# Performance work log

Measured on AMD Instinct MI355X. Metric: run time of the kernel, lower is better.

The kernel has to match this reference:

```python
import math
import jax, jax.numpy as jnp
import numpy as np

B, T, C, FC, H, L, K, WIN = 8, 512, 768, 3072, 12, 6, 3, 4
DK = C // H
SCALE = 1.0 / math.sqrt(DK)


def setup_inputs() -> dict:
    key = jax.random.key(0)
    ks = jax.random.split(key, 12)
    s = 0.02
    rn = lambda k, shape: (jax.random.normal(k, shape, jnp.float32) * s)
    rel_std = DK ** -0.5
    return {
        "x": jax.random.normal(ks[0], (B, C, T), jnp.float32),
        "x_mask": jnp.ones((B, 1, T), jnp.float32),
        "Wq": rn(ks[1], (L, C, C)), "bq": jnp.zeros((L, C), jnp.float32),
        "Wk": rn(ks[2], (L, C, C)), "bk": jnp.zeros((L, C), jnp.float32),
        "Wv": rn(ks[3], (L, C, C)), "bv": jnp.zeros((L, C), jnp.float32),
        "Wo": rn(ks[4], (L, C, C)), "bo": jnp.zeros((L, C), jnp.float32),
        "emb_rel_k": jax.random.normal(ks[5], (1, 2 * WIN + 1, DK), jnp.float32) * rel_std,
        "emb_rel_v": jax.random.normal(ks[6], (1, 2 * WIN + 1, DK), jnp.float32) * rel_std,
        "W1": rn(ks[7], (L, FC, C, K)), "b1": jnp.zeros((L, FC), jnp.float32),
        "W2": rn(ks[8], (L, C, FC, K)), "b2": jnp.zeros((L, C), jnp.float32),
        "g1": jnp.ones((L, C), jnp.float32), "be1": jnp.zeros((L, C), jnp.float32),
        "g2": jnp.ones((L, C), jnp.float32), "be2": jnp.zeros((L, C), jnp.float32),
    }


def _get_rel_emb(emb, length):
    pad = max(length - (WIN + 1), 0)
    start = max(WIN + 1 - length, 0)
    e = jnp.pad(emb, ((0, 0), (pad, pad), (0, 0)))
    return e[:, start:start + 2 * length - 1]


def _rel_to_abs(x):
    # [b,h,l,2l-1] -> [b,h,l,l]
    b, h, l, _ = x.shape
    x = jnp.pad(x, ((0, 0), (0, 0), (0, 0), (0, 1)))
    xf = x.reshape(b, h, l * 2 * l)
    xf = jnp.pad(xf, ((0, 0), (0, 0), (0, l - 1)))
    return xf.reshape(b, h, l + 1, 2 * l - 1)[:, :, :l, l - 1:]


def _abs_to_rel(x):
    # [b,h,l,l] -> [b,h,l,2l-1]
    b, h, l, _ = x.shape
    x = jnp.pad(x, ((0, 0), (0, 0), (0, 0), (0, l - 1)))
    xf = x.reshape(b, h, l * l + l * (l - 1))
    xf = jnp.pad(xf, ((0, 0), (0, 0), (l, 0)))
    return xf.reshape(b, h, l, 2 * l)[:, :, :, 1:]


def _ln(x, g, b):
    # LayerNorm over channel dim of [B,C,T]
    m = jnp.mean(x, axis=1, keepdims=True)
    v = jnp.mean(jnp.square(x - m), axis=1, keepdims=True)
    return (x - m) * jax.lax.rsqrt(v + 1e-5) * g[None, :, None] + b[None, :, None]


def _proj(x, w, b):
    # 1x1 conv == matmul over channels: x [B,C,T], w [O,C]
    return jnp.einsum('oc,bct->bot', w, x) + b[None, :, None]


def _conv1d_same(x, w, b):
    # x [B,Cin,T], w [Cout,Cin,K], same padding (pad_l=(K-1)//2, pad_r=K//2)
    k = w.shape[-1]
    out = jax.lax.conv_general_dilated(
        x, w, window_strides=(1,), padding=[((k - 1) // 2, k // 2)],
        dimension_numbers=('NCH', 'OIH', 'NCH'))
    return out + b[None, :, None]


def _heads(t):
    # [B,C,T] -> [B,H,T,DK]
    return t.reshape(B, H, DK, T).transpose(0, 1, 3, 2)


def _forward(x, x_mask, Wq, bq, Wk, bk, Wv, bv, Wo, bo, emb_rel_k, emb_rel_v,
             W1, b1, W2, b2, g1, be1, g2, be2):
    attn_mask = x_mask[:, :, None, :] * x_mask[:, :, :, None]  # [B,1,T,T]
    x = x * x_mask
    rk = _get_rel_emb(emb_rel_k, T)[0]  # [2T-1, DK]
    rv = _get_rel_emb(emb_rel_v, T)[0]
    for i in range(L):
        # --- self-attention with relative position (matmul + skew) ---
        q = _heads(_proj(x, Wq[i], bq[i]))  # [B,H,T,DK]
        k = _heads(_proj(x, Wk[i], bk[i]))
        v = _heads(_proj(x, Wv[i], bv[i]))
        qs = q * SCALE
        scores = jnp.einsum('bhtd,bhsd->bhts', qs, k)
        rel_logits = jnp.einsum('bhtd,md->bhtm', qs, rk)  # [B,H,T,2T-1]
        scores = scores + _rel_to_abs(rel_logits)
        scores = jnp.where(attn_mask == 0, -1e4, scores)
        p = jax.nn.softmax(scores, axis=-1)
        out = jnp.einsum('bhts,bhsd->bhtd', p, v)
        out = out + jnp.einsum('bhtm,md->bhtd', _abs_to_rel(p), rv)
        out = out.transpose(0, 1, 3, 2).reshape(B, C, T)
        y = _proj(out, Wo[i], bo[i])
        x = _ln(x + y, g1[i], be1[i])
        # --- conv FFN ---
        h = jax.nn.relu(_conv1d_same(x * x_mask, W1[i], b1[i]))
        y = _conv1d_same(h * x_mask, W2[i], b2[i]) * x_mask
        x = _ln(x + y, g2[i], be2[i])
    return x * x_mask


def reference(x, x_mask, Wq, bq, Wk, bk, Wv, bv, Wo, bo, emb_rel_k, emb_rel_v,
              W1, b1, W2, b2, g1, be1, g2, be2):
    return _forward(x, x_mask, Wq, bq, Wk, bk, Wv, bv, Wo, bo, emb_rel_k,
                    emb_rel_v, W1, b1, W2, b2, g1, be1, g2, be2)
```

## Files before the change

### kernel.cpp

```cpp
#include <hip/hip_runtime.h>
#include <stdint.h>

#define L_  6
#define B_  8
#define T_  512
#define C_  768
#define FC_ 3072
#define H_  12
#define DK_ 64
#define TP_ 514
#define QKV_ (3 * C_)

typedef _Float16 half_t;
typedef half_t f16x8 __attribute__((ext_vector_type(8)));
typedef float  f32x4 __attribute__((ext_vector_type(4)));

static constexpr long alg(long x) { return (x + 255) & ~255L; }
constexpr long SLAB = (long)B_ * T_ * C_;

constexpr long SZ_WQKV_B = (long)L_ * QKV_ * C_ * 2;
constexpr long SZ_WO_B   = (long)L_ * C_ * C_ * 2;
constexpr long SZ_W1_B   = (long)L_ * 3 * FC_ * C_ * 2;
constexpr long SZ_BQ_B   = (long)L_ * QKV_ * 4;
constexpr long SZ_ACT_B  = (long)B_ * TP_ * C_ * 2;
constexpr long SZ_VT_B   = ((long)B_ * C_ * T_ + 65536) * 2;
constexpr long SZ_H_B    = (long)B_ * TP_ * FC_ * 2;
constexpr long SZ_P_B    = (long)B_ * H_ * T_ * T_ * 2;
constexpr long SZ_XW_B   = SLAB * 4;
constexpr long SZ_Y_B    = 4 * SLAB * 4;

constexpr long O_WQKV = 0;
constexpr long O_WO  = O_WQKV + alg(SZ_WQKV_B);
constexpr long O_W1  = O_WO   + alg(SZ_WO_B);
constexpr long O_W2  = O_W1   + alg(SZ_W1_B);
constexpr long O_BQ  = O_W2   + alg(SZ_W1_B);
constexpr long O_X   = O_BQ   + alg(SZ_BQ_B);
constexpr long O_Q   = O_X    + alg(SZ_ACT_B);
constexpr long O_K   = O_Q    + alg(SZ_ACT_B);
constexpr long O_ATT = O_K    + alg(SZ_ACT_B);
constexpr long O_VT  = O_ATT  + alg(SZ_ACT_B);
constexpr long O_H   = O_VT   + alg(SZ_VT_B);
constexpr long O_P   = O_H    + alg(SZ_H_B);
constexpr long O_XW  = O_P    + alg(SZ_P_B);
constexpr long O_Y   = O_XW   + alg(SZ_XW_B);
constexpr long WS_NEED = O_Y + alg(SZ_Y_B);

__device__ __forceinline__ void async_ld16(half_t* lds, const half_t* g) {
  __builtin_amdgcn_global_load_lds(
      (const __attribute__((address_space(1))) void*)g,
      (__attribute__((address_space(3))) void*)lds,
      16, 0, 0);
}

struct GemmArgs {
  const half_t* A; const half_t* B; const float* bias;
  void* out; void* out2; void* out3;
  long lda, ldb, ldo;
  long sAz, sAh, sBz, sBh, sBs, sOz, sOh, sPart;
  int hdiv, rowA, rowB, Kc, nshift, ksplit, mode, relu, nlim;
};

__global__ __launch_bounds__(256) void gemm_nt(GemmArgs g) {
  __shared__ half_t As[128 * 32];
  __shared__ half_t Bs[128 * 32];
  const int tid  = threadIdx.x;
  const int lane = tid & 63;
  const int wv   = tid >> 6;
  const int wm   = (wv >> 1) * 64;
  const int wn   = (wv & 1) * 64;
  const int zz   = blockIdx.z;
  const int ks   = zz % g.ksplit;
  const int z    = zz / g.ksplit;
  const int bz   = z / g.hdiv, hz = z % g.hdiv;
  const half_t* Ab = g.A + (long)bz * g.sAz + (long)hz * g.sAh;
  const half_t* Bb = g.B + (long)bz * g.sBz + (long)hz * g.sBh;
  const long m0 = (long)blockIdx.x * 128;
  const long n0 = (long)blockIdx.y * 128;

  const int srow = lane >> 2;
  const int scol = ((((lane & 3) - (srow & 3)) & 3)) * 8;
  half_t* AsW = As + wv * 1024;
  half_t* BsW = Bs + wv * 1024;

  f32x4 acc[4][4];
#pragma unroll
  for (int i = 0; i < 4; ++i)
#pragma unroll
    for (int j = 0; j < 4; ++j) acc[i][j] = f32x4{0.f, 0.f, 0.f, 0.f};

  const int nkb = g.Kc >> 5;
  const int nIter = g.nshift * nkb;
  const int chunk = (nIter + g.ksplit - 1) / g.ksplit;
  int it = ks * chunk;
  const int itEnd0 = it + chunk;
  const int itEnd = itEnd0 < nIter ? itEnd0 : nIter;

  const int kqr = lane >> 4;
  while (it < itEnd) {
    const int s = it / nkb;
    int kbi = it - s * nkb;
    int kbiEnd = kbi + (itEnd - it);
    if (kbiEnd > nkb) kbiEnd = nkb;
    it += kbiEnd - kbi;
    const half_t* Arow = Ab + ((long)(g.rowA + s) + m0) * g.lda;
    const half_t* Brow = Bb + (long)s * g.sBs + (g.rowB + n0) * g.ldb;
    for (; kbi < kbiEnd; ++kbi) {
      const int kb = kbi << 5;
#pragma unroll
      for (int i = 0; i < 2; ++i) {
        async_ld16(AsW + i * 512,
                   Arow + (long)(wv * 32 + i * 16 + srow) * g.lda + kb + scol);
        async_ld16(BsW + i * 512,
                   Brow + (long)(wv * 32 + i * 16 + srow) * g.ldb + kb + scol);
      }
      __syncthreads();
      f16x8 af[4], bfr[4];
#pragma unroll
      for (int f = 0; f < 4; ++f) {
        int rA = wm + f * 16 + (lane & 15);
        int rB = wn + f * 16 + (lane & 15);
        af[f]  = *(const f16x8*)(As + (rA >> 5) * 1024 + (rA & 31) * 32 + ((kqr + rA) & 3) * 8);
        bfr[f] = *(const f16x8*)(Bs + (rB >> 5) * 1024 + (rB & 31) * 32 + ((kqr + rB) & 3) * 8);
      }
#pragma unroll
      for (int fm = 0; fm < 4; ++fm)
#pragma unroll
        for (int fn = 0; fn < 4; ++fn)
          acc[fm][fn] = __builtin_amdgcn_mfma_f32_16x16x32_f16(af[fm], bfr[fn], acc[fm][fn], 0, 0, 0);
      __syncthreads();
    }
  }

  const int col = lane & 15, quad = lane >> 4;
  const long obase = (long)bz * g.sOz + (long)hz * g.sOh + (long)ks * g.sPart;
#pragma unroll
  for (int fm = 0; fm < 4; ++fm) {
#pragma unroll
    for (int fn = 0; fn < 4; ++fn) {
      int n = (int)n0 + wn + fn * 16 + col;
      if (n >= g.nlim) continue;
      float bia = (g.bias && ks == 0) ? g.bias[n] : 0.f;
#pragma unroll
      for (int i = 0; i < 4; ++i) {
        long m = m0 + wm + fm * 16 + quad * 4 + i;
        float v = acc[fm][fn][i] + bia;
        if (g.relu) v = fmaxf(v, 0.f);
        if (g.mode == 0) {
          ((float*)g.out)[obase + m * g.ldo + n] = v;
        } else if (g.mode == 1) {
          ((half_t*)g.out)[obase + m * g.ldo + n] = (half_t)v;
        } else {
          int seg = n / C_, nn = n - seg * C_;
          if (seg == 2)
            ((half_t*)g.out3)[((long)bz * C_ + nn) * T_ + m] = (half_t)v;
          else {
            half_t* dstb = seg ? (half_t*)g.out2 : (half_t*)g.out;
            dstb[((long)bz * TP_ + 1 + m) * C_ + nn] = (half_t)v;
          }
        }
      }
    }
  }
}

__global__ __launch_bounds__(256) void softmax_rel(half_t* p, const half_t* q, const float* erk) {
  const int t = blockIdx.x, h = blockIdx.y, b = blockIdx.z;
  __shared__ float relv[9];
  __shared__ float red[4];
  const int tid = threadIdx.x;
  if (tid < 64) {
    float qv = (float)q[((long)b * TP_ + t + 1) * C_ + h * 64 + tid];
#pragma unroll
    for (int r = 0; r < 9; ++r) {
      float pr = qv * erk[r * 64 + tid];
#pragma unroll
      for (int off = 32; off; off >>= 1) pr += __shfl_xor(pr, off);
      if (tid == 0) relv[r] = pr;
    }
  }
  __syncthreads();
  half_t* row = p + ((long)(b * H_ + h) * T_ + t) * T_;
  float v0 = (float)row[tid], v1 = (float)row[tid + 256];
  int d0 = tid - t + 4, d1 = tid + 256 - t + 4;
  if (d0 >= 0 && d0 < 9) v0 += relv[d0];
  if (d1 >= 0 && d1 < 9) v1 += relv[d1];
  float mx = fmaxf(v0, v1);
#pragma unroll
  for (int off = 32; off; off >>= 1) mx = fmaxf(mx, __shfl_xor(mx, off));
  const int w = tid >> 6;
  if ((tid & 63) == 0) red[w] = mx;
  __syncthreads();
  mx = fmaxf(fmaxf(red[0], red[1]), fmaxf(red[2], red[3]));
  float e0 = __expf(v0 - mx), e1 = __expf(v1 - mx);
  float sm = e0 + e1;
#pragma unroll
  for (int off = 32; off; off >>= 1) sm += __shfl_xor(sm, off);
  __syncthreads();
  if ((tid & 63) == 0) red[w] = sm;
  __syncthreads();
  float inv = 1.f / (red[0] + red[1] + red[2] + red[3]);
  row[tid]       = (half_t)(e0 * inv);
  row[tid + 256] = (half_t)(e1 * inv);
}

__global__ __launch_bounds__(256) void add_rel_v(half_t* attn, const float* pv,
                                                 const half_t* p, const float* erv) {
  const int w = threadIdx.x >> 6, lane = threadIdx.x & 63;
  const int t = blockIdx.x * 4 + w, h = blockIdx.y, b = blockIdx.z;
  const half_t* prow = p + ((long)(b * H_ + h) * T_ + t) * T_;
  long i32 = ((long)b * T_ + t) * C_ + h * 64 + lane;
  float acc = pv[i32] + pv[SLAB + i32];
#pragma unroll
  for (int r = 0; r < 9; ++r) {
    int s = t + r - 4;
    if (s >= 0 && s < T_) acc += (float)prow[s] * erv[r * 64 + lane];
  }
  attn[((long)b * TP_ + t + 1) * C_ + h * 64 + lane] = (half_t)acc;
}

__global__ __launch_bounds__(256) void ln_res(float* xw, const float* yb,
                                              const float* gamma, const float* beta, half_t* xbf) {
  __shared__ float redA[4], redB[4];
  const int row = blockIdx.x;
  const int b = row >> 9, t = row & 511;
  const long base = (long)row * C_;
  float v[3]; float sum = 0.f, sq = 0.f;
#pragma unroll
  for (int i = 0; i < 3; ++i) {
    int c = threadIdx.x + i * 256;
    float s = xw[base + c];
#pragma unroll
    for (int j = 0; j < 4; ++j) s += yb[j * SLAB + base + c];
    v[i] = s; sum += s; sq += s * s;
  }
#pragma unroll
  for (int off = 32; off; off >>= 1) { sum += __shfl_xor(sum, off); sq += __shfl_xor(sq, off); }
  const int w = threadIdx.x >> 6;
  if ((threadIdx.x & 63) == 0) { redA[w] = sum; redB[w] = sq; }
  __syncthreads();
  sum = redA[0] + redA[1] + redA[2] + redA[3];
  sq  = redB[0] + redB[1] + redB[2] + redB[3];
  float mean = sum * (1.f / C_);
  float var  = sq * (1.f / C_) - mean * mean;
  float rstd = rsqrtf(var + 1e-5f);
  const long bb = ((long)b * TP_ + t + 1) * C_;
#pragma unroll
  for (int i = 0; i < 3; ++i) {
    int c = threadIdx.x + i * 256;
    float o = (v[i] - mean) * rstd * gamma[c] + beta[c];
    xw[base + c] = o;
    xbf[bb + c] = (half_t)o;
  }
}

__global__ __launch_bounds__(256) void transpose_in(const float* xin, const float* mask,
                                                    float* xw, half_t* xbf) {
  __shared__ float tl[32][33];
  const int b = blockIdx.z, t0 = blockIdx.x * 32, c0 = blockIdx.y * 32;
  const int tx = threadIdx.x, ty = threadIdx.y;
#pragma unroll
  for (int j = 0; j < 4; ++j) {
    int c = c0 + ty + j * 8;
    tl[ty + j * 8][tx] = xin[((long)b * C_ + c) * T_ + t0 + tx] * mask[(long)b * T_ + t0 + tx];
  }
  __syncthreads();
#pragma unroll
  for (int j = 0; j < 4; ++j) {
    int t = t0 + ty + j * 8;
    float v = tl[tx][ty + j * 8];
    xw[((long)b * T_ + t) * C_ + c0 + tx] = v;
    xbf[((long)b * TP_ + t + 1) * C_ + c0 + tx] = (half_t)v;
  }
}

__global__ __launch_bounds__(256) void transpose_out(const float* xw, const float* mask, float* out) {
  __shared__ float tl[32][33];
  const int b = blockIdx.z, t0 = blockIdx.x * 32, c0 = blockIdx.y * 32;
  const int tx = threadIdx.x, ty = threadIdx.y;
#pragma unroll
  for (int j = 0; j < 4; ++j) {
    int t = t0 + ty + j * 8;
    tl[ty + j * 8][tx] = xw[((long)b * T_ + t) * C_ + c0 + tx];
  }
  __syncthreads();
#pragma unroll
  for (int j = 0; j < 4; ++j) {
    int c = c0 + ty + j * 8;
    out[((long)b * C_ + c) * T_ + t0 + tx] = tl[tx][ty + j * 8] * mask[(long)b * T_ + t0 + tx];
  }
}

__global__ void cvt_f2h(const float* in, half_t* out, long n) {
  long i = (long)blockIdx.x * 256 + threadIdx.x;
  if (i < n) out[i] = (half_t)in[i];
}
__global__ void cvt_wqkv(const float* wq, const float* wk, const float* wv, half_t* out) {
  long i = (long)blockIdx.x * 256 + threadIdx.x;
  const long n = (long)L_ * QKV_ * C_;
  if (i >= n) return;
  long c = i % C_, o = (i / C_) % QKV_, l = i / ((long)QKV_ * C_);
  int seg = (int)(o / C_); long oo = o - (long)seg * C_;
  const float* src = seg == 0 ? wq : (seg == 1 ? wk : wv);
  float v = src[(l * C_ + oo) * C_ + c];
  out[i] = (half_t)(seg == 0 ? v * 0.125f : v);
}
__global__ void cvt_bqkv(const float* bq, const float* bk, const float* bv, float* out) {
  long i = (long)blockIdx.x * 256 + threadIdx.x;
  const long n = (long)L_ * QKV_;
  if (i >= n) return;
  long o = i % QKV_, l = i / QKV_;
  int seg = (int)(o / C_); long oo = o - (long)seg * C_;
  const float* src = seg == 0 ? bq : (seg == 1 ? bk : bv);
  float v = src[l * C_ + oo];
  out[i] = seg == 0 ? v * 0.125f : v;
}
__global__ void cvt_w1(const float* in, half_t* out) {
  long i = (long)blockIdx.x * 256 + threadIdx.x;
  const long n = (long)L_ * 3 * FC_ * C_;
  if (i >= n) return;
  long c = i % C_, f = (i / C_) % FC_, k = (i / ((long)C_ * FC_)) % 3, l = i / (3L * C_ * FC_);
  out[i] = (half_t)in[((l * FC_ + f) * C_ + c) * 3 + k];
}
__global__ void cvt_w2(const float* in, half_t* out) {
  long i = (long)blockIdx.x * 256 + threadIdx.x;
  const long n = (long)L_ * 3 * C_ * FC_;
  if (i >= n) return;
  long f = i % FC_, c = (i / FC_) % C_, k = (i / ((long)FC_ * C_)) % 3, l = i / (3L * FC_ * C_);
  out[i] = (half_t)in[((l * C_ + c) * FC_ + f) * 3 + k];
}
__global__ void zero_pads(half_t* xbf, half_t* hbf) {
  long i = (long)blockIdx.x * 256 + threadIdx.x;
  const long nx = (long)B_ * 2 * C_, nh = (long)B_ * 2 * FC_;
  if (i < nx) {
    long b = i / (2 * C_), r = (i / C_) % 2, c = i % C_;
    xbf[(b * TP_ + (r ? TP_ - 1 : 0)) * C_ + c] = (half_t)0.f;
  } else if (i < nx + nh) {
    long j = i - nx;
    long b = j / (2 * FC_), r = (j / FC_) % 2, f = j % FC_;
    hbf[(b * TP_ + (r ? TP_ - 1 : 0)) * FC_ + f] = (half_t)0.f;
  }
}

extern "C" void kernel_launch(void* const* d_in, const int* in_sizes, int n_in,
                              void* d_out, int out_size, void* d_ws, size_t ws_size,
                              hipStream_t stream) {
  if ((long)ws_size < WS_NEED) return;

  const float* x_in = (const float*)d_in[0];
  const float* mask = (const float*)d_in[1];
  const float* Wq = (const float*)d_in[2];  const float* bq = (const float*)d_in[3];
  const float* Wk = (const float*)d_in[4];  const float* bk = (const float*)d_in[5];
  const float* Wv = (const float*)d_in[6];  const float* bv = (const float*)d_in[7];
  const float* Wo = (const float*)d_in[8];  const float* bo = (const float*)d_in[9];
  const float* erk = (const float*)d_in[10];
  const float* erv = (const float*)d_in[11];
  const float* W1 = (const float*)d_in[12]; const float* b1 = (const float*)d_in[13];
  const float* W2 = (const float*)d_in[14]; const float* b2 = (const float*)d_in[15];
  const float* g1 = (const float*)d_in[16]; const float* be1 = (const float*)d_in[17];
  const float* g2 = (const float*)d_in[18]; const float* be2 = (const float*)d_in[19];

  char* w = (char*)d_ws;
  half_t* wqkv_h = (half_t*)(w + O_WQKV);
  half_t* wo_h = (half_t*)(w + O_WO);
  half_t* w1_h = (half_t*)(w + O_W1);
  half_t* w2_h = (half_t*)(w + O_W2);
  float*  bqkv = (float*)(w + O_BQ);
  half_t* x_h  = (half_t*)(w + O_X);
  half_t* q_h  = (half_t*)(w + O_Q);
  half_t* k_h  = (half_t*)(w + O_K);
  half_t* at_h = (half_t*)(w + O_ATT);
  half_t* vt_h = (half_t*)(w + O_VT);
  half_t* h_h  = (half_t*)(w + O_H);
  half_t* p_h  = (half_t*)(w + O_P);
  float*  xw   = (float*)(w + O_XW);
  float*  yb   = (float*)(w + O_Y);

  const long NWQ = (long)L_ * QKV_ * C_;
  const long NWO = (long)L_ * C_ * C_;
  const long NW1 = (long)L_ * 3 * FC_ * C_;
  cvt_wqkv<<<dim3((NWQ + 255) / 256), 256, 0, stream>>>(Wq, Wk, Wv, wqkv_h);
  cvt_bqkv<<<dim3(((long)L_ * QKV_ + 255) / 256), 256, 0, stream>>>(bq, bk, bv, bqkv);
  cvt_f2h<<<dim3((NWO + 255) / 256), 256, 0, stream>>>(Wo, wo_h, NWO);
  cvt_w1<<<dim3((NW1 + 255) / 256), 256, 0, stream>>>(W1, w1_h);
  cvt_w2<<<dim3((NW1 + 255) / 256), 256, 0, stream>>>(W2, w2_h);
  transpose_in<<<dim3(16, 24, 8), dim3(32, 8), 0, stream>>>(x_in, mask, xw, x_h);
  zero_pads<<<dim3((B_ * 2 * (C_ + FC_) + 255) / 256), 256, 0, stream>>>(x_h, h_h);

  for (int l = 0; l < L_; ++l) {
    GemmArgs a;
    a.out2 = nullptr; a.out3 = nullptr; a.sPart = 0;

    a.A = x_h; a.lda = C_; a.rowA = 1; a.sAz = (long)TP_ * C_; a.sAh = 0;
    a.B = wqkv_h + (long)l * QKV_ * C_; a.ldb = C_; a.rowB = 0; a.sBz = 0; a.sBh = 0; a.sBs = 0;
    a.Kc = C_; a.nshift = 1; a.ksplit = 1; a.bias = bqkv + (long)l * QKV_; a.relu = 0;
    a.out = (void*)q_h; a.out2 = (void*)k_h; a.out3 = (void*)vt_h;
    a.mode = 3; a.ldo = 0; a.sOz = 0; a.sOh = 0;
    a.hdiv = 1; a.nlim = QKV_;
    gemm_nt<<<dim3(4, 18, 8), 256, 0, stream>>>(a);

    a.A = q_h; a.lda = C_; a.rowA = 1; a.sAz = (long)TP_ * C_; a.sAh = 64;
    a.B = k_h; a.ldb = C_; a.rowB = 1; a.sBz = (long)TP_ * C_; a.sBh = 64; a.sBs = 0;
    a.Kc = 64; a.nshift = 1; a.ksplit = 1; a.bias = nullptr; a.relu = 0;
    a.out = (void*)p_h; a.mode = 1; a.ldo = T_;
    a.sOz = (long)H_ * T_ * T_; a.sOh = (long)T_ * T_; a.sPart = 0;
    a.hdiv = H_; a.nlim = T_;
    gemm_nt<<<dim3(4, 4, 96), 256, 0, stream>>>(a);

    softmax_rel<<<dim3(512, 12, 8), 256, 0, stream>>>(p_h, q_h, erk);

    a.A = p_h; a.lda = T_; a.rowA = 0; a.sAz = (long)H_ * T_ * T_; a.sAh = (long)T_ * T_;
    a.B = vt_h; a.ldb = T_; a.rowB = 0; a.sBz = (long)C_ * T_; a.sBh = 64L * T_; a.sBs = 0;
    a.Kc = T_; a.nshift = 1; a.ksplit = 2; a.bias = nullptr; a.relu = 0;
    a.out = (void*)yb; a.mode = 0; a.ldo = C_;
    a.sOz = (long)T_ * C_; a.sOh = 64; a.sPart = SLAB;
    a.hdiv = H_; a.nlim = 64;
    gemm_nt<<<dim3(4, 1, 192), 256, 0, stream>>>(a);

    add_rel_v<<<dim3(128, 12, 8), 256, 0, stream>>>(at_h, yb, p_h, erv);

    a.A = at_h; a.lda = C_; a.rowA = 1; a.sAz = (long)TP_ * C_; a.sAh = 0;
    a.B = wo_h + (long)l * C_ * C_; a.ldb = C_; a.rowB = 0; a.sBz = 0; a.sBh = 0; a.sBs = 0;
    a.Kc = C_; a.nshift = 1; a.ksplit = 4; a.bias = bo + (long)l * C_; a.relu = 0;
    a.out = (void*)yb; a.mode = 0; a.ldo = C_; a.sOz = (long)T_ * C_; a.sOh = 0; a.sPart = SLAB;
    a.hdiv = 1; a.nlim = C_;
    gemm_nt<<<dim3(4, 6, 32), 256, 0, stream>>>(a);

    ln_res<<<dim3(B_ * T_), 256, 0, stream>>>(xw, yb, g1 + (long)l * C_, be1 + (long)l * C_, x_h);

    a.A = x_h; a.lda = C_; a.rowA = 0; a.sAz = (long)TP_ * C_; a.sAh = 0;
    a.B = w1_h + (long)l * 3 * FC_ * C_; a.ldb = C_; a.rowB = 0; a.sBz = 0; a.sBh = 0;
    a.sBs = (long)FC_ * C_;
    a.Kc = C_; a.nshift = 3; a.ksplit = 1; a.bias = b1 + (long)l * FC_; a.relu = 1;
    a.out = (void*)(h_h + FC_); a.mode = 1; a.ldo = FC_; a.sOz = (long)TP_ * FC_; a.sOh = 0; a.sPart = 0;
    a.hdiv = 1; a.nlim = FC_;
    gemm_nt<<<dim3(4, 24, 8), 256, 0, stream>>>(a);

    a.A = h_h; a.lda = FC_; a.rowA = 0; a.sAz = (long)TP_ * FC_; a.sAh = 0;
    a.B = w2_h + (long)l * 3 * C_ * FC_; a.ldb = FC_; a.rowB = 0; a.sBz = 0; a.sBh = 0;
    a.sBs = (long)C_ * FC_;
    a.Kc = FC_; a.nshift = 3; a.ksplit = 4; a.bias = b2 + (long)l * C_; a.relu = 0;
    a.out = (void*)yb; a.mode = 0; a.ldo = C_; a.sOz = (long)T_ * C_; a.sOh = 0; a.sPart = SLAB;
    a.hdiv = 1; a.nlim = C_;
    gemm_nt<<<dim3(4, 6, 32), 256, 0, stream>>>(a);

    ln_res<<<dim3(B_ * T_), 256, 0, stream>>>(xw, yb, g2 + (long)l * C_, be2 + (long)l * C_, x_h);
  }

  transpose_out<<<dim3(16, 24, 8), dim3(32, 8), 0, stream>>>(xw, mask, (float*)d_out);
}
```

Measured before the change: 3.111 ms.

## Fuse attention into flash-style kernel with banded relative-position correction

Replaces the QK^T GEMM, the softmax with relative-key bias, and the PV GEMM with a single flash-attention kernel. It uses MFMA, keeps an online softmax and never writes the full B*H*T*T probability matrix to global memory. The relative-key logits are computed per block with MFMA against the 9-entry embedding and added inside the band. A separate band kernel recomputes the 9 banded probabilities from the saved row max and sum and adds the relative-value term. This removes large score-matrix traffic and several launches, at the cost of extra LDS use, lower occupancy and only 384 blocks in the fused kernel.

```diff
diff --git a/kernel.cpp b/kernel.cpp
--- a/kernel.cpp
+++ b/kernel.cpp
@@ -25,7 +25,7 @@
 constexpr long SZ_ACT_B  = (long)B_ * TP_ * C_ * 2;
 constexpr long SZ_VT_B   = ((long)B_ * C_ * T_ + 65536) * 2;
 constexpr long SZ_H_B    = (long)B_ * TP_ * FC_ * 2;
-constexpr long SZ_P_B    = (long)B_ * H_ * T_ * T_ * 2;
+constexpr long SZ_ML_B   = 2L * B_ * H_ * T_ * 4;
 constexpr long SZ_XW_B   = SLAB * 4;
 constexpr long SZ_Y_B    = 4 * SLAB * 4;
 
@@ -40,8 +40,8 @@
 constexpr long O_ATT = O_K    + alg(SZ_ACT_B);
 constexpr long O_VT  = O_ATT  + alg(SZ_ACT_B);
 constexpr long O_H   = O_VT   + alg(SZ_VT_B);
-constexpr long O_P   = O_H    + alg(SZ_H_B);
-constexpr long O_XW  = O_P    + alg(SZ_P_B);
+constexpr long O_ML  = O_H    + alg(SZ_H_B);
+constexpr long O_XW  = O_ML   + alg(SZ_ML_B);
 constexpr long O_Y   = O_XW   + alg(SZ_XW_B);
 constexpr long WS_NEED = O_Y + alg(SZ_Y_B);
 
@@ -163,59 +163,206 @@
   }
 }
 
-__global__ __launch_bounds__(256) void softmax_rel(half_t* p, const half_t* q, const float* erk) {
-  const int t = blockIdx.x, h = blockIdx.y, b = blockIdx.z;
-  __shared__ float relv[9];
-  __shared__ float red[4];
-  const int tid = threadIdx.x;
-  if (tid < 64) {
-    float qv = (float)q[((long)b * TP_ + t + 1) * C_ + h * 64 + tid];
-#pragma unroll
-    for (int r = 0; r < 9; ++r) {
-      float pr = qv * erk[r * 64 + tid];
-#pragma unroll
-      for (int off = 32; off; off >>= 1) pr += __shfl_xor(pr, off);
-      if (tid == 0) relv[r] = pr;
-    }
-  }
-  __syncthreads();
-  half_t* row = p + ((long)(b * H_ + h) * T_ + t) * T_;
-  float v0 = (float)row[tid], v1 = (float)row[tid + 256];
-  int d0 = tid - t + 4, d1 = tid + 256 - t + 4;
-  if (d0 >= 0 && d0 < 9) v0 += relv[d0];
-  if (d1 >= 0 && d1 < 9) v1 += relv[d1];
-  float mx = fmaxf(v0, v1);
-#pragma unroll
-  for (int off = 32; off; off >>= 1) mx = fmaxf(mx, __shfl_xor(mx, off));
-  const int w = tid >> 6;
-  if ((tid & 63) == 0) red[w] = mx;
-  __syncthreads();
-  mx = fmaxf(fmaxf(red[0], red[1]), fmaxf(red[2], red[3]));
-  float e0 = __expf(v0 - mx), e1 = __expf(v1 - mx);
-  float sm = e0 + e1;
-#pragma unroll
-  for (int off = 32; off; off >>= 1) sm += __shfl_xor(sm, off);
-  __syncthreads();
-  if ((tid & 63) == 0) red[w] = sm;
-  __syncthreads();
-  float inv = 1.f / (red[0] + red[1] + red[2] + red[3]);
-  row[tid]       = (half_t)(e0 * inv);
-  row[tid + 256] = (half_t)(e1 * inv);
-}
-
-__global__ __launch_bounds__(256) void add_rel_v(half_t* attn, const float* pv,
-                                                 const half_t* p, const float* erv) {
+__global__ __launch_bounds__(256) void attn_fused(
+    const half_t* __restrict__ q, const half_t* __restrict__ k,
+    const half_t* __restrict__ vt, const float* __restrict__ erk,
+    half_t* __restrict__ attn, float* __restrict__ m_ws, float* __restrict__ l_ws) {
+  __shared__ half_t Ks[128 * 64];
+  __shared__ half_t Vs[64 * 128];
+  __shared__ half_t Ps[4][32 * 132];
+  __shared__ float  rl[4][32][12];
+
+  const int tid = threadIdx.x, lane = tid & 63, w = tid >> 6;
+  const int h = blockIdx.y, b = blockIdx.z;
+  const int q0 = blockIdx.x * 128;
+  const int l15 = lane & 15, quad = lane >> 4;
+  const long hbase = ((long)b * TP_ + 1) * C_ + h * 64;
+
+  f16x8 qa[2][2];
+#pragma unroll
+  for (int fm = 0; fm < 2; ++fm)
+#pragma unroll
+    for (int kf = 0; kf < 2; ++kf) {
+      int t = q0 + w * 32 + fm * 16 + l15;
+      qa[fm][kf] = *(const f16x8*)(q + hbase + (long)t * C_ + kf * 32 + quad * 8);
+    }
+
+  {
+    f16x8 eb[2];
+#pragma unroll
+    for (int kf = 0; kf < 2; ++kf) {
+      f16x8 e;
+#pragma unroll
+      for (int j = 0; j < 8; ++j)
+        e[j] = (half_t)(l15 < 9 ? erk[l15 * 64 + kf * 32 + quad * 8 + j] : 0.f);
+      eb[kf] = e;
+    }
+#pragma unroll
+    for (int fm = 0; fm < 2; ++fm) {
+      f32x4 a = f32x4{0.f, 0.f, 0.f, 0.f};
+      a = __builtin_amdgcn_mfma_f32_16x16x32_f16(qa[fm][0], eb[0], a, 0, 0, 0);
+      a = __builtin_amdgcn_mfma_f32_16x16x32_f16(qa[fm][1], eb[1], a, 0, 0, 0);
+      if (l15 < 9)
+#pragma unroll
+        for (int i = 0; i < 4; ++i)
+          rl[w][fm * 16 + quad * 4 + i][l15] = a[i];
+    }
+  }
+
+  float mst[2][4], lst[2][4];
+  f32x4 Oa[2][4];
+#pragma unroll
+  for (int fm = 0; fm < 2; ++fm)
+#pragma unroll
+    for (int i = 0; i < 4; ++i) { mst[fm][i] = -1e30f; lst[fm][i] = 0.f; }
+#pragma unroll
+  for (int fm = 0; fm < 2; ++fm)
+#pragma unroll
+    for (int fn = 0; fn < 4; ++fn) Oa[fm][fn] = f32x4{0.f, 0.f, 0.f, 0.f};
+
+  for (int kt = 0; kt < 4; ++kt) {
+    const int s0 = kt * 128;
+    __syncthreads();
+#pragma unroll
+    for (int i = 0; i < 4; ++i) {
+      int row = w * 32 + i * 8 + (lane >> 3);
+      int sl = ((lane & 7) - row) & 7;
+      async_ld16(Ks + (w * 32 + i * 8) * 64,
+                 k + hbase + (long)(s0 + row) * C_ + sl * 8);
+    }
+#pragma unroll
+    for (int i = 0; i < 4; ++i) {
+      int d = w * 16 + i * 4 + (lane >> 4);
+      int sl = ((lane & 15) - d) & 15;
+      async_ld16(Vs + (w * 16 + i * 4) * 128,
+                 vt + ((long)b * C_ + h * 64 + d) * T_ + s0 + sl * 8);
+    }
+    __syncthreads();
+
+    f32x4 Sa[2][8];
+#pragma unroll
+    for (int fm = 0; fm < 2; ++fm)
+#pragma unroll
+      for (int fn = 0; fn < 8; ++fn) Sa[fm][fn] = f32x4{0.f, 0.f, 0.f, 0.f};
+#pragma unroll
+    for (int ks = 0; ks < 2; ++ks)
+#pragma unroll
+      for (int fn = 0; fn < 8; ++fn) {
+        int row = fn * 16 + l15;
+        int p = ((ks * 4 + quad) + row) & 7;
+        f16x8 bf = *(const f16x8*)(Ks + row * 64 + p * 8);
+        Sa[0][fn] = __builtin_amdgcn_mfma_f32_16x16x32_f16(qa[0][ks], bf, Sa[0][fn], 0, 0, 0);
+        Sa[1][fn] = __builtin_amdgcn_mfma_f32_16x16x32_f16(qa[1][ks], bf, Sa[1][fn], 0, 0, 0);
+      }
+
+#pragma unroll
+    for (int fm = 0; fm < 2; ++fm) {
+      int rbase = q0 + w * 32 + fm * 16;
+#pragma unroll
+      for (int fn = 0; fn < 8; ++fn) {
+        int db = s0 + fn * 16 - rbase + 4;
+        if (db < -15 || db > 23) continue;
+#pragma unroll
+        for (int i = 0; i < 4; ++i) {
+          int d = db + l15 - quad * 4 - i;
+          if (d >= 0 && d < 9)
+            Sa[fm][fn][i] += rl[w][fm * 16 + quad * 4 + i][d];
+        }
+      }
+    }
+
+#pragma unroll
+    for (int fm = 0; fm < 2; ++fm) {
+      float tmax[4] = {-1e30f, -1e30f, -1e30f, -1e30f};
+#pragma unroll
+      for (int fn = 0; fn < 8; ++fn)
+#pragma unroll
+        for (int i = 0; i < 4; ++i) tmax[i] = fmaxf(tmax[i], Sa[fm][fn][i]);
+#pragma unroll
+      for (int i = 0; i < 4; ++i) {
+#pragma unroll
+        for (int off = 1; off < 16; off <<= 1)
+          tmax[i] = fmaxf(tmax[i], __shfl_xor(tmax[i], off));
+      }
+      float alpha[4], rsum[4];
+#pragma unroll
+      for (int i = 0; i < 4; ++i) {
+        float mn = fmaxf(mst[fm][i], tmax[i]);
+        alpha[i] = __expf(mst[fm][i] - mn);
+        mst[fm][i] = mn;
+        rsum[i] = 0.f;
+      }
+#pragma unroll
+      for (int fn = 0; fn < 8; ++fn)
+#pragma unroll
+        for (int i = 0; i < 4; ++i) {
+          float e = __expf(Sa[fm][fn][i] - mst[fm][i]);
+          rsum[i] += e;
+          Ps[w][(fm * 16 + quad * 4 + i) * 132 + fn * 16 + l15] = (half_t)e;
+        }
+#pragma unroll
+      for (int i = 0; i < 4; ++i) {
+#pragma unroll
+        for (int off = 1; off < 16; off <<= 1) rsum[i] += __shfl_xor(rsum[i], off);
+        lst[fm][i] = lst[fm][i] * alpha[i] + rsum[i];
+#pragma unroll
+        for (int fn2 = 0; fn2 < 4; ++fn2) Oa[fm][fn2][i] *= alpha[i];
+      }
+    }
+
+#pragma unroll
+    for (int ks2 = 0; ks2 < 4; ++ks2) {
+      f16x8 pa[2];
+#pragma unroll
+      for (int fm = 0; fm < 2; ++fm)
+        pa[fm] = *(const f16x8*)(&Ps[w][(fm * 16 + l15) * 132 + ks2 * 32 + quad * 8]);
+#pragma unroll
+      for (int fn2 = 0; fn2 < 4; ++fn2) {
+        int d = fn2 * 16 + l15;
+        int p = ((ks2 * 4 + quad) + d) & 15;
+        f16x8 bv = *(const f16x8*)(Vs + d * 128 + p * 8);
+        Oa[0][fn2] = __builtin_amdgcn_mfma_f32_16x16x32_f16(pa[0], bv, Oa[0][fn2], 0, 0, 0);
+        Oa[1][fn2] = __builtin_amdgcn_mfma_f32_16x16x32_f16(pa[1], bv, Oa[1][fn2], 0, 0, 0);
+      }
+    }
+  }
+
+  const long mlbase = ((long)b * H_ + h) * T_;
+#pragma unroll
+  for (int fm = 0; fm < 2; ++fm)
+#pragma unroll
+    for (int i = 0; i < 4; ++i) {
+      int t = q0 + w * 32 + fm * 16 + quad * 4 + i;
+      float inv = 1.f / lst[fm][i];
+      if (l15 == 0) { m_ws[mlbase + t] = mst[fm][i]; l_ws[mlbase + t] = lst[fm][i]; }
+#pragma unroll
+      for (int fn2 = 0; fn2 < 4; ++fn2)
+        attn[hbase + (long)t * C_ + fn2 * 16 + l15] = (half_t)(Oa[fm][fn2][i] * inv);
+    }
+}
+
+__global__ __launch_bounds__(256) void band_rel_v(
+    half_t* attn, const half_t* q, const half_t* k, const float* erk,
+    const float* erv, const float* m_ws, const float* l_ws) {
   const int w = threadIdx.x >> 6, lane = threadIdx.x & 63;
   const int t = blockIdx.x * 4 + w, h = blockIdx.y, b = blockIdx.z;
-  const half_t* prow = p + ((long)(b * H_ + h) * T_ + t) * T_;
-  long i32 = ((long)b * T_ + t) * C_ + h * 64 + lane;
-  float acc = pv[i32] + pv[SLAB + i32];
+  const long base = ((long)b * TP_ + 1 + t) * C_ + h * 64 + lane;
+  const float qv = (float)q[base];
+  const long ml = ((long)b * H_ + h) * T_ + t;
+  const float m = m_ws[ml];
+  const float inv = 1.f / l_ws[ml];
+  float acc = 0.f;
 #pragma unroll
   for (int r = 0; r < 9; ++r) {
     int s = t + r - 4;
-    if (s >= 0 && s < T_) acc += (float)prow[s] * erv[r * 64 + lane];
-  }
-  attn[((long)b * TP_ + t + 1) * C_ + h * 64 + lane] = (half_t)acc;
+    if (s < 0 || s >= T_) continue;
+    float kv = (float)k[((long)b * TP_ + 1 + s) * C_ + h * 64 + lane];
+    float dot = qv * (kv + erk[r * 64 + lane]);
+#pragma unroll
+    for (int off = 32; off; off >>= 1) dot += __shfl_xor(dot, off);
+    acc += __expf(dot - m) * inv * erv[r * 64 + lane];
+  }
+  attn[base] = (half_t)((float)attn[base] + acc);
 }
 
 __global__ __launch_bounds__(256) void ln_res(float* xw, const float* yb,
@@ -371,7 +518,8 @@
   half_t* at_h = (half_t*)(w + O_ATT);
   half_t* vt_h = (half_t*)(w + O_VT);
   half_t* h_h  = (half_t*)(w + O_H);
-  half_t* p_h  = (half_t*)(w + O_P);
+  float*  m_ws = (float*)(w + O_ML);
+  float*  l_ws = m_ws + (long)B_ * H_ * T_;
   float*  xw   = (float*)(w + O_XW);
   float*  yb   = (float*)(w + O_Y);
 
@@ -398,26 +546,11 @@
     a.hdiv = 1; a.nlim = QKV_;
     gemm_nt<<<dim3(4, 18, 8), 256, 0, stream>>>(a);
 
-    a.A = q_h; a.lda = C_; a.rowA = 1; a.sAz = (long)TP_ * C_; a.sAh = 64;
-    a.B = k_h; a.ldb = C_; a.rowB = 1; a.sBz = (long)TP_ * C_; a.sBh = 64; a.sBs = 0;
-    a.Kc = 64; a.nshift = 1; a.ksplit = 1; a.bias = nullptr; a.relu = 0;
-    a.out = (void*)p_h; a.mode = 1; a.ldo = T_;
-    a.sOz = (long)H_ * T_ * T_; a.sOh = (long)T_ * T_; a.sPart = 0;
-    a.hdiv = H_; a.nlim = T_;
-    gemm_nt<<<dim3(4, 4, 96), 256, 0, stream>>>(a);
-
-    softmax_rel<<<dim3(512, 12, 8), 256, 0, stream>>>(p_h, q_h, erk);
-
-    a.A = p_h; a.lda = T_; a.rowA = 0; a.sAz = (long)H_ * T_ * T_; a.sAh = (long)T_ * T_;
-    a.B = vt_h; a.ldb = T_; a.rowB = 0; a.sBz = (long)C_ * T_; a.sBh = 64L * T_; a.sBs = 0;
-    a.Kc = T_; a.nshift = 1; a.ksplit = 2; a.bias = nullptr; a.relu = 0;
-    a.out = (void*)yb; a.mode = 0; a.ldo = C_;
-    a.sOz = (long)T_ * C_; a.sOh = 64; a.sPart = SLAB;
-    a.hdiv = H_; a.nlim = 64;
-    gemm_nt<<<dim3(4, 1, 192), 256, 0, stream>>>(a);
-
-    add_rel_v<<<dim3(128, 12, 8), 256, 0, stream>>>(at_h, yb, p_h, erv);
-
+    attn_fused<<<dim3(4, H_, B_), 256, 0, stream>>>(q_h, k_h, vt_h, erk, at_h, m_ws, l_ws);
+
+    band_rel_v<<<dim3(128, H_, B_), 256, 0, stream>>>(at_h, q_h, k_h, erk, erv, m_ws, l_ws);
+
+    a.out2 = nullptr; a.out3 = nullptr;
     a.A = at_h; a.lda = C_; a.rowA = 1; a.sAz = (long)TP_ * C_; a.sAh = 0;
     a.B = wo_h + (long)l * C_ * C_; a.ldb = C_; a.rowB = 0; a.sBz = 0; a.sBh = 0; a.sBs = 0;
     a.Kc = C_; a.nshift = 1; a.ksplit = 4; a.bias = bo + (long)l * C_; a.relu = 0;
```

Result: faster. 2.524 ms (-18.9%).
